# Kernel optimization log

Measured on AMD Instinct MI355X. Metric: run time of the kernel, lower is better.

The kernel has to match this reference:

```python
import jax, jax.numpy as jnp
import numpy as np

REG = 0.01          # regularisation (target epsilon)
DECAY = 0.9         # decay_rate
MIN_UPDATE = 0.01   # min_update_size
MAX_ITERS = 50      # max_iterations
GRAD_CLIP = 1.0     # transport_gradient_clip
B, N, D = 4, 2048, 16


@jax.custom_vjp
def clip_grad_identity(t):
    # identity fwd; clips the cotangent of the transport matrix in bwd
    return t

def _cg_fwd(t):
    return t, None

def _cg_bwd(_, dt):
    return (jnp.clip(dt, -GRAD_CLIP, GRAD_CLIP),)

clip_grad_identity.defvjp(_cg_fwd, _cg_bwd)


def _diameter(x):
    # max over dims of per-sample std (ddof=0), per batch -> (B,1)
    d = jnp.max(jnp.std(x, axis=1), axis=-1, keepdims=True)
    return jnp.where(d == 0.0, jnp.ones_like(d), d)


def _sq_cdist(x):
    # squared euclidean auto-distance matrix, (B,N,N)
    sq = jnp.sum(x * x, axis=-1)
    c = sq[:, :, None] + sq[:, None, :] - 2.0 * jnp.einsum('bnd,bmd->bnm', x, x)
    return jnp.maximum(c, 0.0)


def sinkhorn_loop(log_a, log_b, cost, eps_target, min_update, max_iter, eps0, rate):
    """Log-domain Sinkhorn with per-batch exponentially decayed epsilon and
    masked early stopping (data-dependent stop expressed as a convergence mask
    so the loop is jit/vjp friendly). eps0: (B,1,1) initial regularisation
    (extent of the scaled particles, per Thornton & Corenflos)."""
    Bb, _ = log_a.shape
    init = (jnp.zeros_like(log_a), jnp.zeros_like(log_b), eps0,
            jnp.zeros((Bb, 1), dtype=bool))

    @jax.checkpoint
    def step(carry, _):
        f, g, eps, done = carry              # eps: (B,1,1), done: (B,1)
        eps2 = eps[:, :, 0]                  # (B,1)
        # f_i = -eps * LSE_j( log_b_j + (g_j - C_ij)/eps )
        f_new = -eps2 * jax.nn.logsumexp(log_b[:, None, :] + (g[:, None, :] - cost) / eps, axis=-1)
        cT = jnp.swapaxes(cost, 1, 2)
        # g_j = -eps * LSE_i( log_a_i + (f_i - C_ij)/eps )
        g_new = -eps2 * jax.nn.logsumexp(log_a[:, None, :] + (f_new[:, None, :] - cT) / eps, axis=-1)
        upd = jnp.maximum(jnp.max(jnp.abs(f_new - f), axis=-1),
                          jnp.max(jnp.abs(g_new - g), axis=-1))[:, None]  # (B,1)
        converged = (upd < min_update) & (eps2 <= eps_target)
        f = jnp.where(done, f, f_new)
        g = jnp.where(done, g, g_new)
        eps = jnp.where(done[:, :, None], eps, jnp.maximum(eps * rate, eps_target))
        done = done | converged
        return (f, g, eps, done), None

    (f, g, eps, _), _ = jax.lax.scan(step, init, None, length=max_iter)
    return f, g, eps


def _forward(state, weight):
    n = state.shape[1]
    log_b = jnp.full(weight.shape, -jnp.log(float(n)), weight.dtype)  # log uniform
    centred = state - jax.lax.stop_gradient(jnp.mean(state, axis=1, keepdims=True))
    scale = jax.lax.stop_gradient(_diameter(state)) * jnp.sqrt(float(state.shape[-1]))  # (B,1)
    sx = centred / scale[:, :, None]
    cost = _sq_cdist(sx)                                              # (B,N,N)
    extent = (jnp.max(sx, axis=(1, 2)) - jnp.min(sx, axis=(1, 2))).reshape(-1, 1, 1)
    f, g, _ = sinkhorn_loop(weight, log_b, cost, REG, MIN_UPDATE, MAX_ITERS, extent, DECAY)
    # transport from potentials at the target regularisation
    log_T = weight[:, :, None] + log_b[:, None, :] + (f[:, :, None] + g[:, None, :] - cost) / REG
    transport = clip_grad_identity(jnp.exp(log_T))                    # (B,N,N)
    # new particle m = N * sum_n T_nm x_n
    new_state = float(n) * jnp.einsum('bnm,bnd->bmd', transport, state)
    return new_state


def setup_inputs() -> dict:
    key = jax.random.key(0)
    k1, k2 = jax.random.split(key)
    state = jax.random.normal(k1, (B, N, D), dtype=jnp.float32)
    weight = jax.nn.log_softmax(jax.random.normal(k2, (B, N), dtype=jnp.float32), axis=-1)
    return {"state": state, "weight": weight}


def reference(state, weight):
    new_state = _forward(state, weight)
    uniform_log_w = jnp.full(weight.shape, -jnp.log(float(weight.shape[1])), weight.dtype)
    return (new_state, uniform_log_w)
```

## Files before the change

kernel.cpp:

```cpp
#include <hip/hip_runtime.h>

#define BATCH 4
#define NPTS  2048
#define DIM   16
#define REGEPS 0.01f
#define DECAYF 0.9f
#define MINUPD 0.01f
#define MAXIT  50
#define LOGN   7.62461898616f
#define L2E    1.44269504089f
#define LN2    0.69314718056f

typedef float v2f __attribute__((ext_vector_type(2)));

#define OFF_SX    0
#define OFF_SQ    (BATCH*NPTS*DIM)
#define OFF_F     (OFF_SQ + BATCH*NPTS)
#define OFF_G     (OFF_F + BATCH*NPTS)
#define OFF_MEAN  (OFF_G + BATCH*NPTS)
#define OFF_SCALE (OFF_MEAN + BATCH*DIM)
#define OFF_EPS0  (OFF_SCALE + BATCH)
#define OFF_SYNC  155776

__global__ __launch_bounds__(256) void ot_preproc(const float* __restrict__ state,
                                                  float* __restrict__ ws) {
  const int b = blockIdx.x;
  const int tid = threadIdx.x;
  __shared__ float s_sum[16][17];
  __shared__ float s_sq[16][17];
  __shared__ float s_mean[16];
  __shared__ float s_red[8];
  __shared__ float s_scale_sh;

  const float* st = state + b * NPTS * DIM;
  const int d = tid & 15, grp = tid >> 4;
  float sm = 0.f, s2 = 0.f;
  for (int n = grp; n < NPTS; n += 16) {
    float x = st[n * DIM + d];
    sm += x; s2 += x * x;
  }
  s_sum[grp][d] = sm; s_sq[grp][d] = s2;
  __syncthreads();
  if (tid < 16) {
    float S = 0.f, Q = 0.f;
    for (int g2 = 0; g2 < 16; ++g2) { S += s_sum[g2][tid]; Q += s_sq[g2][tid]; }
    float mean = S * (1.0f / NPTS);
    float var  = fmaxf(Q * (1.0f / NPTS) - mean * mean, 0.f);
    float sd   = sqrtf(var);
    s_mean[tid] = mean;
    ws[OFF_MEAN + b * DIM + tid] = mean;
    s_sum[0][tid] = sd;
  }
  __syncthreads();
  if (tid == 0) {
    float dm = 0.f;
    for (int d2 = 0; d2 < 16; ++d2) dm = fmaxf(dm, s_sum[0][d2]);
    if (dm == 0.f) dm = 1.f;
    float scale = dm * 4.0f;
    s_scale_sh = scale;
    ws[OFF_SCALE + b] = scale;
  }
  __syncthreads();

  const float inv_scale = 1.0f / s_scale_sh;
  float vmin = 3.0e38f, vmax = -3.0e38f;
  float* sx = ws + OFF_SX + b * NPTS * DIM;
  float* sq = ws + OFF_SQ + b * NPTS;
  for (int n = tid; n < NPTS; n += 256) {
    const float4* rp = (const float4*)(st + n * DIM);
    float4 xs0 = rp[0], xs1 = rp[1], xs2 = rp[2], xs3 = rp[3];
    float xv[16] = {xs0.x,xs0.y,xs0.z,xs0.w, xs1.x,xs1.y,xs1.z,xs1.w,
                    xs2.x,xs2.y,xs2.z,xs2.w, xs3.x,xs3.y,xs3.z,xs3.w};
    float ov[16];
    float q = 0.f;
    #pragma unroll
    for (int e = 0; e < 16; ++e) {
      float v = (xv[e] - s_mean[e]) * inv_scale;
      ov[e] = v; q += v * v;
      vmin = fminf(vmin, v); vmax = fmaxf(vmax, v);
    }
    float4* op = (float4*)(sx + n * DIM);
    op[0] = make_float4(ov[0],ov[1],ov[2],ov[3]);
    op[1] = make_float4(ov[4],ov[5],ov[6],ov[7]);
    op[2] = make_float4(ov[8],ov[9],ov[10],ov[11]);
    op[3] = make_float4(ov[12],ov[13],ov[14],ov[15]);
    sq[n] = q;
  }
  float* fv = ws + OFF_F + b * NPTS;
  float* gv = ws + OFF_G + b * NPTS;
  for (int n = tid; n < NPTS; n += 256) { fv[n] = 0.f; gv[n] = 0.f; }
  #pragma unroll
  for (int off = 32; off > 0; off >>= 1) {
    vmin = fminf(vmin, __shfl_xor(vmin, off));
    vmax = fmaxf(vmax, __shfl_xor(vmax, off));
  }
  const int wv = tid >> 6, ln = tid & 63;
  if (ln == 0) { s_red[wv] = vmin; s_red[4 + wv] = vmax; }
  __syncthreads();
  if (tid == 0) {
    float mn = fminf(fminf(s_red[0], s_red[1]), fminf(s_red[2], s_red[3]));
    float mx = fmaxf(fmaxf(s_red[4], s_red[5]), fmaxf(s_red[6], s_red[7]));
    ws[OFF_EPS0 + b] = mx - mn;
  }
  int* sy = (int*)ws + OFF_SYNC + b * 128;
  for (int k = tid; k < 128; k += 256) sy[k] = 0;
}

__device__ __forceinline__ float4 load_f4_coherent(const float* p) {
  float4 v;
  asm volatile("global_load_dwordx4 %0, %1, off sc0 sc1\n\t"
               "s_waitcnt vmcnt(0)"
               : "=v"(v) : "v"(p) : "memory");
  return v;
}

__device__ __forceinline__ void batch_barrier(int* sy, int ph) {
  __syncthreads();
  if (threadIdx.x == 0) {
    int* arrive = sy;
    int* epoch  = sy + 32;
    const int old = __hip_atomic_fetch_add(arrive, 1, __ATOMIC_ACQ_REL,
                                           __HIP_MEMORY_SCOPE_AGENT);
    if (old == 64 * ph - 1) {
      __hip_atomic_store(epoch, ph, __ATOMIC_RELEASE, __HIP_MEMORY_SCOPE_AGENT);
    } else {
      while (__hip_atomic_load(epoch, __ATOMIC_RELAXED, __HIP_MEMORY_SCOPE_AGENT) < ph)
        __builtin_amdgcn_s_sleep(2);
      (void)__hip_atomic_load(epoch, __ATOMIC_ACQUIRE, __HIP_MEMORY_SCOPE_AGENT);
    }
  }
  __syncthreads();
}

__device__ __forceinline__ void lse_sweep(const float* __restrict__ s_xt,
                                          const float* __restrict__ s_a2,
                                          const float (&sxr)[4][16],
                                          float inv_eps, int l,
                                          float (&M)[4], float (&S)[4]) {
  const v2f inv2 = { inv_eps, inv_eps };
  #pragma unroll
  for (int r = 0; r < 4; ++r) { M[r] = -3.0e38f; S[r] = 0.0f; }
  for (int c = 0; c < 8; ++c) {
    const int jb = c * 256 + 4 * l;
    const float4 af = *(const float4*)(s_a2 + jb);
    const v2f av0 = { af.x, af.y }, av1 = { af.z, af.w };
    v2f acc[4][2];
    {
      const float4 xf = *(const float4*)(s_xt + jb);
      const v2f x0 = { xf.x, xf.y }, x1 = { xf.z, xf.w };
      #pragma unroll
      for (int r = 0; r < 4; ++r) {
        const v2f sv = { sxr[r][0], sxr[r][0] };
        acc[r][0] = x0 * sv;
        acc[r][1] = x1 * sv;
      }
    }
    #pragma unroll
    for (int dd = 1; dd < 16; ++dd) {
      const float4 xf = *(const float4*)(s_xt + dd * 2048 + jb);
      const v2f x0 = { xf.x, xf.y }, x1 = { xf.z, xf.w };
      #pragma unroll
      for (int r = 0; r < 4; ++r) {
        const v2f sv = { sxr[r][dd], sxr[r][dd] };
        acc[r][0] = __builtin_elementwise_fma(x0, sv, acc[r][0]);
        acc[r][1] = __builtin_elementwise_fma(x1, sv, acc[r][1]);
      }
    }
    #pragma unroll
    for (int r = 0; r < 4; ++r) {
      const v2f v01 = __builtin_elementwise_fma(acc[r][0], inv2, av0);
      const v2f v23 = __builtin_elementwise_fma(acc[r][1], inv2, av1);
      const float v0 = v01.x, v1 = v01.y, v2 = v23.x, v3 = v23.y;
      const float cmx = fmaxf(fmaxf(v0, v1), fmaxf(v2, v3));
      const float nm = fmaxf(M[r], cmx);
      const float e0 = exp2f(M[r] - nm);
      const float sa = exp2f(v0-nm) + exp2f(v1-nm) + exp2f(v2-nm) + exp2f(v3-nm);
      S[r] = fmaf(S[r], e0, sa);
      M[r] = nm;
    }
  }
}

__device__ __forceinline__ void lse_butterfly(float (&M)[4], float (&S)[4]) {
  #pragma unroll
  for (int off = 1; off < 64; off <<= 1) {
    #pragma unroll
    for (int r = 0; r < 4; ++r) {
      const float om = __shfl_xor(M[r], off);
      const float os = __shfl_xor(S[r], off);
      const float nm = fmaxf(M[r], om);
      S[r] = S[r] * exp2f(M[r] - nm) + os * exp2f(om - nm);
      M[r] = nm;
    }
  }
}

__global__ __launch_bounds__(512, 2) void ot_sinkhorn(float* __restrict__ ws,
                                                      const float* __restrict__ wlog) {
  extern __shared__ float lds[];
  float* s_xt  = lds;
  float* s_a2  = lds + 16 * 2048;
  float* s_wl2 = s_a2 + 2048;
  float* s_q   = s_wl2 + 2048;

  const int bid = blockIdx.x;
  const int b  = bid >> 6;
  const int rb = bid & 63;
  const int tid = threadIdx.x;
  const int w = tid >> 6, l = tid & 63;

  const float* __restrict__ sx = ws + OFF_SX + b * NPTS * DIM;
  const float* __restrict__ sq = ws + OFF_SQ + b * NPTS;
  float* fv = ws + OFF_F + b * NPTS;
  float* gv = ws + OFF_G + b * NPTS;
  const float* __restrict__ wl = wlog + b * NPTS;
  int* sy = (int*)ws + OFF_SYNC + b * 128;
  unsigned int* up2 = (unsigned int*)sy + 2;

  for (int j = tid; j < NPTS; j += 512) {
    const float4* rp = (const float4*)(sx + j * DIM);
    float4 t0 = rp[0], t1 = rp[1], t2 = rp[2], t3 = rp[3];
    s_xt[ 0*2048+j]=t0.x; s_xt[ 1*2048+j]=t0.y; s_xt[ 2*2048+j]=t0.z; s_xt[ 3*2048+j]=t0.w;
    s_xt[ 4*2048+j]=t1.x; s_xt[ 5*2048+j]=t1.y; s_xt[ 6*2048+j]=t1.z; s_xt[ 7*2048+j]=t1.w;
    s_xt[ 8*2048+j]=t2.x; s_xt[ 9*2048+j]=t2.y; s_xt[10*2048+j]=t2.z; s_xt[11*2048+j]=t2.w;
    s_xt[12*2048+j]=t3.x; s_xt[13*2048+j]=t3.y; s_xt[14*2048+j]=t3.z; s_xt[15*2048+j]=t3.w;
    s_wl2[j] = wl[j] * L2E;
    s_q[j]   = sq[j];
  }
  const int row0 = rb * 32 + w * 4;
  const float qi_own = (l < 4) ? sq[row0 + l] : 0.f;
  float eps = ws[OFF_EPS0 + b];
  __syncthreads();

  int ph = 0;
  for (int it = 0; it < MAXIT; ++it) {
    const float le      = L2E / eps;
    const float eln2    = eps * LN2;
    const float inv_eps = 1.0f / eps;

    float sxr[4][16];
    {
      const volatile float* vxt = s_xt;
      #pragma unroll
      for (int r = 0; r < 4; ++r)
        #pragma unroll
        for (int dd = 0; dd < 16; ++dd)
          sxr[r][dd] = vxt[dd * 2048 + row0 + r] * (2.0f * L2E);
    }

    {
      const int j4 = tid * 4;
      const float4 g4 = load_f4_coherent(gv + j4);
      const float4 q4 = *(const float4*)(s_q + j4);
      *(float4*)(s_a2 + j4) = make_float4((g4.x - q4.x) * le, (g4.y - q4.y) * le,
                                          (g4.z - q4.z) * le, (g4.w - q4.w) * le);
    }
    __syncthreads();
    {
      float M[4], S[4];
      lse_sweep(s_xt, s_a2, sxr, inv_eps, l, M, S);
      lse_butterfly(M, S);
      if (l < 4) {
        const float Mr = (l==0)?M[0]:(l==1)?M[1]:(l==2)?M[2]:M[3];
        const float Sr = (l==0)?S[0]:(l==1)?S[1]:(l==2)?S[2]:S[3];
        const int i = row0 + l;
        const float fnew = fmaf(eps, LOGN, qi_own) - eln2 * (Mr + log2f(Sr));
        const float old = __hip_atomic_load(fv + i, __ATOMIC_RELAXED, __HIP_MEMORY_SCOPE_AGENT);
        __hip_atomic_store(fv + i, fnew, __ATOMIC_RELEASE, __HIP_MEMORY_SCOPE_AGENT);
        __hip_atomic_fetch_max(up2 + (it & 1), __float_as_uint(fabsf(fnew - old)),
                               __ATOMIC_RELAXED, __HIP_MEMORY_SCOPE_AGENT);
      }
    }
    ++ph; batch_barrier(sy, ph);

    if (rb == 0 && tid == 0)
      __hip_atomic_store(up2 + ((it + 1) & 1), 0u, __ATOMIC_RELAXED, __HIP_MEMORY_SCOPE_AGENT);
    {
      const int j4 = tid * 4;
      const float4 f4 = load_f4_coherent(fv + j4);
      const float4 q4 = *(const float4*)(s_q + j4);
      const float4 w2 = *(const float4*)(s_wl2 + j4);
      *(float4*)(s_a2 + j4) = make_float4(fmaf(f4.x - q4.x, le, w2.x), fmaf(f4.y - q4.y, le, w2.y),
                                          fmaf(f4.z - q4.z, le, w2.z), fmaf(f4.w - q4.w, le, w2.w));
    }
    __syncthreads();
    {
      float M[4], S[4];
      lse_sweep(s_xt, s_a2, sxr, inv_eps, l, M, S);
      lse_butterfly(M, S);
      if (l < 4) {
        const float Mr = (l==0)?M[0]:(l==1)?M[1]:(l==2)?M[2]:M[3];
        const float Sr = (l==0)?S[0]:(l==1)?S[1]:(l==2)?S[2]:S[3];
        const int i = row0 + l;
        const float gnew = qi_own - eln2 * (Mr + log2f(Sr));
        const float old = __hip_atomic_load(gv + i, __ATOMIC_RELAXED, __HIP_MEMORY_SCOPE_AGENT);
        __hip_atomic_store(gv + i, gnew, __ATOMIC_RELEASE, __HIP_MEMORY_SCOPE_AGENT);
        __hip_atomic_fetch_max(up2 + (it & 1), __float_as_uint(fabsf(gnew - old)),
                               __ATOMIC_RELAXED, __HIP_MEMORY_SCOPE_AGENT);
      }
    }
    if (it < MAXIT - 1) {
      ++ph; batch_barrier(sy, ph);
      const unsigned uu = __hip_atomic_load(up2 + (it & 1), __ATOMIC_RELAXED, __HIP_MEMORY_SCOPE_AGENT);
      const bool conv = (__uint_as_float(uu) < MINUPD) && (eps <= REGEPS);
      if (conv) break;
      eps = fmaxf(eps * DECAYF, REGEPS);
    }
  }
}

__global__ __launch_bounds__(256) void ot_out(float* __restrict__ ws,
                                              const float* __restrict__ wlog,
                                              float* __restrict__ out) {
  __shared__ float s_xt[DIM][256];
  __shared__ float s_p[256];
  __shared__ float s_q[256];
  const int bid = blockIdx.x;
  const int b  = bid >> 8;
  const int rb = bid & 255;
  const int tid = threadIdx.x;
  const int w = tid >> 6, l = tid & 63;
  const float invR = 1.0f / REGEPS;

  const float* __restrict__ sx = ws + OFF_SX + b * NPTS * DIM;
  const float* __restrict__ sq = ws + OFF_SQ + b * NPTS;
  const float* __restrict__ fv = ws + OFF_F + b * NPTS;
  const float* __restrict__ gv = ws + OFF_G + b * NPTS;
  const float* __restrict__ wl = wlog + b * NPTS;

  const int row0 = rb * 8 + w * 2;
  float sxm[2][DIM], cm2[2], qm[2], acc[2][DIM], accT[2];
  #pragma unroll
  for (int r = 0; r < 2; ++r) {
    const int mrow = row0 + r;
    cm2[r] = sq[mrow];
    qm[r]  = gv[mrow] * invR;
    const float4* rp = (const float4*)(sx + mrow * DIM);
    #pragma unroll
    for (int c4 = 0; c4 < 4; ++c4) {
      float4 t = rp[c4];
      sxm[r][c4*4+0] = -2.0f * t.x; sxm[r][c4*4+1] = -2.0f * t.y;
      sxm[r][c4*4+2] = -2.0f * t.z; sxm[r][c4*4+3] = -2.0f * t.w;
    }
    #pragma unroll
    for (int dd = 0; dd < DIM; ++dd) acc[r][dd] = 0.0f;
    accT[r] = 0.0f;
  }

  for (int k = 0; k < NPTS / 256; ++k) {
    __syncthreads();
    {
      const int n = k * 256 + tid;
      const float4* rp = (const float4*)(sx + n * DIM);
      float4 t0 = rp[0], t1 = rp[1], t2 = rp[2], t3 = rp[3];
      s_xt[0][tid]=t0.x;  s_xt[1][tid]=t0.y;  s_xt[2][tid]=t0.z;  s_xt[3][tid]=t0.w;
      s_xt[4][tid]=t1.x;  s_xt[5][tid]=t1.y;  s_xt[6][tid]=t1.z;  s_xt[7][tid]=t1.w;
      s_xt[8][tid]=t2.x;  s_xt[9][tid]=t2.y;  s_xt[10][tid]=t2.z; s_xt[11][tid]=t2.w;
      s_xt[12][tid]=t3.x; s_xt[13][tid]=t3.y; s_xt[14][tid]=t3.z; s_xt[15][tid]=t3.w;
      s_q[tid] = sq[n];
      s_p[tid] = wl[n] - LOGN + fv[n] * invR;
    }
    __syncthreads();
    const float4 pv = *(const float4*)&s_p[4 * l];
    const float4 qv = *(const float4*)&s_q[4 * l];
    float a2[2][4];
    #pragma unroll
    for (int r = 0; r < 2; ++r) {
      a2[r][0] = cm2[r] + qv.x; a2[r][1] = cm2[r] + qv.y;
      a2[r][2] = cm2[r] + qv.z; a2[r][3] = cm2[r] + qv.w;
    }
    #pragma unroll
    for (int dd = 0; dd < DIM; ++dd) {
      const float4 xj = *(const float4*)&s_xt[dd][4 * l];
      #pragma unroll
      for (int r = 0; r < 2; ++r) {
        const float xr = sxm[r][dd];
        a2[r][0] = fmaf(xr, xj.x, a2[r][0]);
        a2[r][1] = fmaf(xr, xj.y, a2[r][1]);
        a2[r][2] = fmaf(xr, xj.z, a2[r][2]);
        a2[r][3] = fmaf(xr, xj.w, a2[r][3]);
      }
    }
    float T[2][4];
    #pragma unroll
    for (int r = 0; r < 2; ++r) {
      T[r][0] = __expf(fmaf(fmaxf(a2[r][0], 0.f), -invR, pv.x + qm[r]));
      T[r][1] = __expf(fmaf(fmaxf(a2[r][1], 0.f), -invR, pv.y + qm[r]));
      T[r][2] = __expf(fmaf(fmaxf(a2[r][2], 0.f), -invR, pv.z + qm[r]));
      T[r][3] = __expf(fmaf(fmaxf(a2[r][3], 0.f), -invR, pv.w + qm[r]));
      accT[r] += (T[r][0] + T[r][1]) + (T[r][2] + T[r][3]);
    }
    #pragma unroll
    for (int dd = 0; dd < DIM; ++dd) {
      const float4 xj = *(const float4*)&s_xt[dd][4 * l];
      #pragma unroll
      for (int r = 0; r < 2; ++r) {
        float t = acc[r][dd];
        t = fmaf(T[r][0], xj.x, t);
        t = fmaf(T[r][1], xj.y, t);
        t = fmaf(T[r][2], xj.z, t);
        t = fmaf(T[r][3], xj.w, t);
        acc[r][dd] = t;
      }
    }
  }
  #pragma unroll
  for (int off = 1; off < 64; off <<= 1) {
    #pragma unroll
    for (int r = 0; r < 2; ++r) {
      #pragma unroll
      for (int dd = 0; dd < DIM; ++dd) acc[r][dd] += __shfl_xor(acc[r][dd], off);
      accT[r] += __shfl_xor(accT[r], off);
    }
  }
  if (l == 0) {
    const float scale = ws[OFF_SCALE + b];
    const float* mean = ws + OFF_MEAN + b * DIM;
    #pragma unroll
    for (int r = 0; r < 2; ++r) {
      const int mrow = row0 + r;
      float ov[16];
      #pragma unroll
      for (int dd = 0; dd < DIM; ++dd)
        ov[dd] = (float)NPTS * fmaf(scale, acc[r][dd], mean[dd] * accT[r]);
      float4* op = (float4*)(out + (b * NPTS + mrow) * DIM);
      op[0] = make_float4(ov[0],ov[1],ov[2],ov[3]);
      op[1] = make_float4(ov[4],ov[5],ov[6],ov[7]);
      op[2] = make_float4(ov[8],ov[9],ov[10],ov[11]);
      op[3] = make_float4(ov[12],ov[13],ov[14],ov[15]);
    }
  }
  if (tid < 8) out[BATCH * NPTS * DIM + b * NPTS + rb * 8 + tid] = -LOGN;
}

extern "C" void kernel_launch(void* const* d_in, const int* in_sizes, int n_in,
                              void* d_out, int out_size, void* d_ws, size_t ws_size,
                              hipStream_t stream) {
  (void)in_sizes; (void)n_in; (void)out_size; (void)ws_size;
  const float* state  = (const float*)d_in[0];
  const float* weight = (const float*)d_in[1];
  float* out = (float*)d_out;
  float* ws  = (float*)d_ws;

  ot_preproc<<<dim3(BATCH), dim3(256), 0, stream>>>(state, ws);

  const unsigned int dynLds = (16 * 2048 + 3 * 2048 + 8) * 4;
  (void)hipFuncSetAttribute((const void*)ot_sinkhorn,
                            hipFuncAttributeMaxDynamicSharedMemorySize, (int)dynLds);
  hipLaunchKernelGGL(ot_sinkhorn, dim3(256), dim3(512), dynLds, stream, ws, weight);

  ot_out<<<dim3(BATCH * NPTS / 8), dim3(256), 0, stream>>>(ws, weight, out);
}
```

Baseline: 3.635 ms.

## Split Sinkhorn LSE sweep into 8-row by half-column wave tiles with LDS merge

Each wave now handles 8 rows over half of the columns instead of 4 rows over all columns. Two waves' partial log-sum-exp results are merged through a small LDS buffer, so every loaded column vector feeds twice as many rows. Scaled row coordinates are staged once in LDS instead of being gathered from the transposed layout each iteration. The coherent inline-asm vector load is replaced by relaxed atomic scalar loads, and the convergence atomics are skipped until eps reaches its target. The cost is higher register pressure from the 8x16 row array and an extra block barrier per half-step.

New measurement: 9.912 ms. 2.73x slower.

```diff
diff --git a/kernel.cpp b/kernel.cpp
--- a/kernel.cpp
+++ b/kernel.cpp
@@ -106,14 +106,6 @@
   for (int k = tid; k < 128; k += 256) sy[k] = 0;
 }
 
-__device__ __forceinline__ float4 load_f4_coherent(const float* p) {
-  float4 v;
-  asm volatile("global_load_dwordx4 %0, %1, off sc0 sc1\n\t"
-               "s_waitcnt vmcnt(0)"
-               : "=v"(v) : "v"(p) : "memory");
-  return v;
-}
-
 __device__ __forceinline__ void batch_barrier(int* sy, int ph) {
   __syncthreads();
   if (threadIdx.x == 0) {
@@ -132,24 +124,29 @@
   __syncthreads();
 }
 
-__device__ __forceinline__ void lse_sweep(const float* __restrict__ s_xt,
-                                          const float* __restrict__ s_a2,
-                                          const float (&sxr)[4][16],
-                                          float inv_eps, int l,
-                                          float (&M)[4], float (&S)[4]) {
+__device__ __forceinline__ float sel8(const float (&A)[8], int l) {
+  return (l==0)?A[0]:(l==1)?A[1]:(l==2)?A[2]:(l==3)?A[3]
+        :(l==4)?A[4]:(l==5)?A[5]:(l==6)?A[6]:A[7];
+}
+
+__device__ __forceinline__ void lse_sweep8(const float* __restrict__ s_xt,
+                                           const float* __restrict__ s_a2,
+                                           const float (&sxr)[8][16],
+                                           float inv_eps, int jbase, int l,
+                                           float (&M)[8], float (&S)[8]) {
   const v2f inv2 = { inv_eps, inv_eps };
   #pragma unroll
-  for (int r = 0; r < 4; ++r) { M[r] = -3.0e38f; S[r] = 0.0f; }
-  for (int c = 0; c < 8; ++c) {
-    const int jb = c * 256 + 4 * l;
+  for (int r = 0; r < 8; ++r) { M[r] = -3.0e38f; S[r] = 0.0f; }
+  for (int c = 0; c < 4; ++c) {
+    const int jb = jbase + c * 256 + 4 * l;
     const float4 af = *(const float4*)(s_a2 + jb);
     const v2f av0 = { af.x, af.y }, av1 = { af.z, af.w };
-    v2f acc[4][2];
+    v2f acc[8][2];
     {
       const float4 xf = *(const float4*)(s_xt + jb);
       const v2f x0 = { xf.x, xf.y }, x1 = { xf.z, xf.w };
       #pragma unroll
-      for (int r = 0; r < 4; ++r) {
+      for (int r = 0; r < 8; ++r) {
         const v2f sv = { sxr[r][0], sxr[r][0] };
         acc[r][0] = x0 * sv;
         acc[r][1] = x1 * sv;
@@ -160,14 +157,14 @@
       const float4 xf = *(const float4*)(s_xt + dd * 2048 + jb);
       const v2f x0 = { xf.x, xf.y }, x1 = { xf.z, xf.w };
       #pragma unroll
-      for (int r = 0; r < 4; ++r) {
+      for (int r = 0; r < 8; ++r) {
         const v2f sv = { sxr[r][dd], sxr[r][dd] };
         acc[r][0] = __builtin_elementwise_fma(x0, sv, acc[r][0]);
         acc[r][1] = __builtin_elementwise_fma(x1, sv, acc[r][1]);
       }
     }
     #pragma unroll
-    for (int r = 0; r < 4; ++r) {
+    for (int r = 0; r < 8; ++r) {
       const v2f v01 = __builtin_elementwise_fma(acc[r][0], inv2, av0);
       const v2f v23 = __builtin_elementwise_fma(acc[r][1], inv2, av1);
       const float v0 = v01.x, v1 = v01.y, v2 = v23.x, v3 = v23.y;
@@ -181,11 +178,11 @@
   }
 }
 
-__device__ __forceinline__ void lse_butterfly(float (&M)[4], float (&S)[4]) {
+__device__ __forceinline__ void lse_butterfly8(float (&M)[8], float (&S)[8]) {
   #pragma unroll
   for (int off = 1; off < 64; off <<= 1) {
     #pragma unroll
-    for (int r = 0; r < 4; ++r) {
+    for (int r = 0; r < 8; ++r) {
       const float om = __shfl_xor(M[r], off);
       const float os = __shfl_xor(S[r], off);
       const float nm = fmaxf(M[r], om);
@@ -198,16 +195,20 @@
 __global__ __launch_bounds__(512, 2) void ot_sinkhorn(float* __restrict__ ws,
                                                       const float* __restrict__ wlog) {
   extern __shared__ float lds[];
-  float* s_xt  = lds;
-  float* s_a2  = lds + 16 * 2048;
-  float* s_wl2 = s_a2 + 2048;
-  float* s_q   = s_wl2 + 2048;
+  float* s_xt   = lds;
+  float* s_a2   = lds + 16 * 2048;
+  float* s_wl2  = s_a2 + 2048;
+  float* s_q    = s_wl2 + 2048;
+  float* s_rows = s_q + 2048;
+  float* s_mrg  = s_rows + 512;
 
   const int bid = blockIdx.x;
   const int b  = bid >> 6;
   const int rb = bid & 63;
   const int tid = threadIdx.x;
   const int w = tid >> 6, l = tid & 63;
+  const int wlo = w & 3;
+  const int jbase = (w >> 2) * 1024;
 
   const float* __restrict__ sx = ws + OFF_SX + b * NPTS * DIM;
   const float* __restrict__ sq = ws + OFF_SQ + b * NPTS;
@@ -227,8 +228,12 @@
     s_wl2[j] = wl[j] * L2E;
     s_q[j]   = sq[j];
   }
-  const int row0 = rb * 32 + w * 4;
-  const float qi_own = (l < 4) ? sq[row0 + l] : 0.f;
+  if (tid < 512) {
+    const int row = tid >> 4, dd = tid & 15;
+    s_rows[tid] = sx[(rb * 32 + row) * DIM + dd] * (2.0f * L2E);
+  }
+  const int row0 = rb * 32 + wlo * 8;
+  const float qi_own = (l < 8) ? sq[row0 + l] : 0.f;
   float eps = ws[OFF_EPS0 + b];
   __syncthreads();
 
@@ -237,73 +242,98 @@
     const float le      = L2E / eps;
     const float eln2    = eps * LN2;
     const float inv_eps = 1.0f / eps;
-
-    float sxr[4][16];
-    {
-      const volatile float* vxt = s_xt;
-      #pragma unroll
-      for (int r = 0; r < 4; ++r)
+    const bool  check   = (eps <= REGEPS);
+
+    const int j4 = tid * 4;
+    float e0 = __hip_atomic_load(gv + j4 + 0, __ATOMIC_RELAXED, __HIP_MEMORY_SCOPE_AGENT);
+    float e1 = __hip_atomic_load(gv + j4 + 1, __ATOMIC_RELAXED, __HIP_MEMORY_SCOPE_AGENT);
+    float e2 = __hip_atomic_load(gv + j4 + 2, __ATOMIC_RELAXED, __HIP_MEMORY_SCOPE_AGENT);
+    float e3 = __hip_atomic_load(gv + j4 + 3, __ATOMIC_RELAXED, __HIP_MEMORY_SCOPE_AGENT);
+
+    float sxr[8][16];
+    {
+      const volatile float* vr = s_rows + (wlo * 8) * 16;
+      #pragma unroll
+      for (int r = 0; r < 8; ++r)
         #pragma unroll
         for (int dd = 0; dd < 16; ++dd)
-          sxr[r][dd] = vxt[dd * 2048 + row0 + r] * (2.0f * L2E);
-    }
-
-    {
-      const int j4 = tid * 4;
-      const float4 g4 = load_f4_coherent(gv + j4);
+          sxr[r][dd] = vr[r * 16 + dd];
+    }
+    {
       const float4 q4 = *(const float4*)(s_q + j4);
-      *(float4*)(s_a2 + j4) = make_float4((g4.x - q4.x) * le, (g4.y - q4.y) * le,
-                                          (g4.z - q4.z) * le, (g4.w - q4.w) * le);
+      *(float4*)(s_a2 + j4) = make_float4((e0 - q4.x) * le, (e1 - q4.y) * le,
+                                          (e2 - q4.z) * le, (e3 - q4.w) * le);
     }
     __syncthreads();
     {
-      float M[4], S[4];
-      lse_sweep(s_xt, s_a2, sxr, inv_eps, l, M, S);
-      lse_butterfly(M, S);
-      if (l < 4) {
-        const float Mr = (l==0)?M[0]:(l==1)?M[1]:(l==2)?M[2]:M[3];
-        const float Sr = (l==0)?S[0]:(l==1)?S[1]:(l==2)?S[2]:S[3];
+      float M[8], S[8];
+      lse_sweep8(s_xt, s_a2, sxr, inv_eps, jbase, l, M, S);
+      lse_butterfly8(M, S);
+      if (w >= 4 && l < 8) {
+        s_mrg[(wlo * 8 + l) * 2]     = sel8(M, l);
+        s_mrg[(wlo * 8 + l) * 2 + 1] = sel8(S, l);
+      }
+      __syncthreads();
+      if (w < 4 && l < 8) {
+        const float M1 = sel8(M, l), S1 = sel8(S, l);
+        const float M2 = s_mrg[(wlo * 8 + l) * 2];
+        const float S2 = s_mrg[(wlo * 8 + l) * 2 + 1];
+        const float nm = fmaxf(M1, M2);
+        const float St = S1 * exp2f(M1 - nm) + S2 * exp2f(M2 - nm);
         const int i = row0 + l;
-        const float fnew = fmaf(eps, LOGN, qi_own) - eln2 * (Mr + log2f(Sr));
+        const float fnew = fmaf(eps, LOGN, qi_own) - eln2 * (nm + log2f(St));
         const float old = __hip_atomic_load(fv + i, __ATOMIC_RELAXED, __HIP_MEMORY_SCOPE_AGENT);
         __hip_atomic_store(fv + i, fnew, __ATOMIC_RELEASE, __HIP_MEMORY_SCOPE_AGENT);
-        __hip_atomic_fetch_max(up2 + (it & 1), __float_as_uint(fabsf(fnew - old)),
-                               __ATOMIC_RELAXED, __HIP_MEMORY_SCOPE_AGENT);
+        if (check)
+          __hip_atomic_fetch_max(up2 + (it & 1), __float_as_uint(fabsf(fnew - old)),
+                                 __ATOMIC_RELAXED, __HIP_MEMORY_SCOPE_AGENT);
       }
     }
     ++ph; batch_barrier(sy, ph);
 
     if (rb == 0 && tid == 0)
       __hip_atomic_store(up2 + ((it + 1) & 1), 0u, __ATOMIC_RELAXED, __HIP_MEMORY_SCOPE_AGENT);
-    {
-      const int j4 = tid * 4;
-      const float4 f4 = load_f4_coherent(fv + j4);
+    e0 = __hip_atomic_load(fv + j4 + 0, __ATOMIC_RELAXED, __HIP_MEMORY_SCOPE_AGENT);
+    e1 = __hip_atomic_load(fv + j4 + 1, __ATOMIC_RELAXED, __HIP_MEMORY_SCOPE_AGENT);
+    e2 = __hip_atomic_load(fv + j4 + 2, __ATOMIC_RELAXED, __HIP_MEMORY_SCOPE_AGENT);
+    e3 = __hip_atomic_load(fv + j4 + 3, __ATOMIC_RELAXED, __HIP_MEMORY_SCOPE_AGENT);
+    {
       const float4 q4 = *(const float4*)(s_q + j4);
       const float4 w2 = *(const float4*)(s_wl2 + j4);
-      *(float4*)(s_a2 + j4) = make_float4(fmaf(f4.x - q4.x, le, w2.x), fmaf(f4.y - q4.y, le, w2.y),
-                                          fmaf(f4.z - q4.z, le, w2.z), fmaf(f4.w - q4.w, le, w2.w));
+      *(float4*)(s_a2 + j4) = make_float4(fmaf(e0 - q4.x, le, w2.x), fmaf(e1 - q4.y, le, w2.y),
+                                          fmaf(e2 - q4.z, le, w2.z), fmaf(e3 - q4.w, le, w2.w));
     }
     __syncthreads();
     {
-      float M[4], S[4];
-      lse_sweep(s_xt, s_a2, sxr, inv_eps, l, M, S);
-      lse_butterfly(M, S);
-      if (l < 4) {
-        const float Mr = (l==0)?M[0]:(l==1)?M[1]:(l==2)?M[2]:M[3];
-        const float Sr = (l==0)?S[0]:(l==1)?S[1]:(l==2)?S[2]:S[3];
+      float M[8], S[8];
+      lse_sweep8(s_xt, s_a2, sxr, inv_eps, jbase, l, M, S);
+      lse_butterfly8(M, S);
+      if (w >= 4 && l < 8) {
+        s_mrg[(wlo * 8 + l) * 2]     = sel8(M, l);
+        s_mrg[(wlo * 8 + l) * 2 + 1] = sel8(S, l);
+      }
+      __syncthreads();
+      if (w < 4 && l < 8) {
+        const float M1 = sel8(M, l), S1 = sel8(S, l);
+        const float M2 = s_mrg[(wlo * 8 + l) * 2];
+        const float S2 = s_mrg[(wlo * 8 + l) * 2 + 1];
+        const float nm = fmaxf(M1, M2);
+        const float St = S1 * exp2f(M1 - nm) + S2 * exp2f(M2 - nm);
         const int i = row0 + l;
-        const float gnew = qi_own - eln2 * (Mr + log2f(Sr));
+        const float gnew = qi_own - eln2 * (nm + log2f(St));
         const float old = __hip_atomic_load(gv + i, __ATOMIC_RELAXED, __HIP_MEMORY_SCOPE_AGENT);
         __hip_atomic_store(gv + i, gnew, __ATOMIC_RELEASE, __HIP_MEMORY_SCOPE_AGENT);
-        __hip_atomic_fetch_max(up2 + (it & 1), __float_as_uint(fabsf(gnew - old)),
-                               __ATOMIC_RELAXED, __HIP_MEMORY_SCOPE_AGENT);
+        if (check)
+          __hip_atomic_fetch_max(up2 + (it & 1), __float_as_uint(fabsf(gnew - old)),
+                                 __ATOMIC_RELAXED, __HIP_MEMORY_SCOPE_AGENT);
       }
     }
     if (it < MAXIT - 1) {
       ++ph; batch_barrier(sy, ph);
-      const unsigned uu = __hip_atomic_load(up2 + (it & 1), __ATOMIC_RELAXED, __HIP_MEMORY_SCOPE_AGENT);
-      const bool conv = (__uint_as_float(uu) < MINUPD) && (eps <= REGEPS);
-      if (conv) break;
+      if (check) {
+        const unsigned uu = __hip_atomic_load(up2 + (it & 1), __ATOMIC_RELAXED, __HIP_MEMORY_SCOPE_AGENT);
+        if (__uint_as_float(uu) < MINUPD) break;
+      }
       eps = fmaxf(eps * DECAYF, REGEPS);
     }
   }
@@ -444,7 +474,7 @@
 
   ot_preproc<<<dim3(BATCH), dim3(256), 0, stream>>>(state, ws);
 
-  const unsigned int dynLds = (16 * 2048 + 3 * 2048 + 8) * 4;
+  const unsigned int dynLds = (16 * 2048 + 3 * 2048 + 512 + 64) * 4;
   (void)hipFuncSetAttribute((const void*)ot_sinkhorn,
                             hipFuncAttributeMaxDynamicSharedMemorySize, (int)dynLds);
   hipLaunchKernelGGL(ot_sinkhorn, dim3(256), dim3(512), dynLds, stream, ws, weight);
```
